# Performance work log

Measured on AMD Instinct MI355X. Metric: run time of the kernel, lower is better.

The kernel has to match this reference:

```python
import jax, jax.numpy as jnp
import numpy as np

B, T, D = 4, 256, 256
H, DK = 4, 64
NUM_REL = 64
EPS = 1e-5


def setup_inputs() -> dict:
    key = jax.random.key(0)
    ks = jax.random.split(key, 16)
    s = 0.02
    return {
        "node_features": jax.random.normal(ks[0], (B, T, D), jnp.float32),
        "spatial_matrix": jax.random.randint(ks[1], (B, T, T), 0, NUM_REL, jnp.int32),
        "Wq": jax.random.normal(ks[2], (D, D), jnp.float32) * s,
        "bq": jnp.zeros((D,), jnp.float32),
        "Wk": jax.random.normal(ks[3], (D, D), jnp.float32) * s,
        "bk": jnp.zeros((D,), jnp.float32),
        "Wv": jax.random.normal(ks[4], (D, D), jnp.float32) * s,
        "bv": jnp.zeros((D,), jnp.float32),
        "rel_k": jax.random.normal(ks[5], (NUM_REL, D), jnp.float32) * s,
        "rel_v": jax.random.normal(ks[6], (NUM_REL, D), jnp.float32) * s,
        "Wo": jax.random.normal(ks[7], (D, D), jnp.float32) * s,
        "bo": jnp.zeros((D,), jnp.float32),
        "gamma": jnp.ones((D,), jnp.float32),
        "beta": jnp.zeros((D,), jnp.float32),
    }


def reference(node_features, spatial_matrix, Wq, bq, Wk, bk, Wv, bv,
              rel_k, rel_v, Wo, bo, gamma, beta):
    b, t, d = node_features.shape
    # projections -> [B,T,H,dk]
    q = (node_features @ Wq.T + bq).reshape(b, t, H, DK)
    k = (node_features @ Wk.T + bk).reshape(b, t, H, DK)
    v = (node_features @ Wv.T + bv).reshape(b, t, H, DK)
    # per-edge relation embeddings -> [B,T,T,H,dk]
    r_k = rel_k[spatial_matrix].reshape(b, t, t, H, DK)
    r_v = rel_v[spatial_matrix].reshape(b, t, t, H, DK)
    # k' = k_j + r_{ij}; scores[b,i,j,h] = <q_i, k'_{ij}> / sqrt(dk)
    k_prime = k[:, None, :, :, :] + r_k
    scores = jnp.einsum('bihd,bijhd->bijh', q, k_prime) / jnp.sqrt(jnp.float32(DK))
    attn = jax.nn.softmax(scores, axis=2)  # over key index j (dropout p used in eval => identity)
    v_prime = v[:, None, :, :, :] + r_v
    agg = jnp.einsum('bijh,bijhd->bihd', attn, v_prime).reshape(b, t, d)
    out = agg @ Wo.T + bo + node_features
    # LayerNorm over last dim
    mu = jnp.mean(out, axis=-1, keepdims=True)
    var = jnp.var(out, axis=-1, keepdims=True)
    out = (out - mu) / jnp.sqrt(var + EPS) * gamma + beta
    return jax.nn.relu(out)
```

## Files before the change

kernel.cpp:

```cpp
#include <hip/hip_runtime.h>

#define TT 256
#define DD 256
#define NH 4
#define DKK 64
#define NR 64
#define NB 4

#define FMA4(A, S, V) { A.x += (S)*(V).x; A.y += (S)*(V).y; A.z += (S)*(V).z; A.w += (S)*(V).w; }

__global__ __launch_bounds__(256) void k_qkv(
    const float* __restrict__ x,
    const float* __restrict__ Wq, const float* __restrict__ bq,
    const float* __restrict__ Wk, const float* __restrict__ bk,
    const float* __restrict__ Wv, const float* __restrict__ bv,
    float* __restrict__ Q, float* __restrict__ K, float* __restrict__ V)
{
    const int z = blockIdx.z;
    const float* __restrict__ W    = (z == 0) ? Wq : (z == 1) ? Wk : Wv;
    const float* __restrict__ bias = (z == 0) ? bq : (z == 1) ? bk : bv;
    float* __restrict__ out        = (z == 0) ? Q  : (z == 1) ? K  : V;
    const int r0 = blockIdx.x * 16, c0 = blockIdx.y * 64;
    __shared__ float xl[16][68];
    __shared__ float wl[64][68];
    const int t = threadIdx.x;
    const int cg = t & 15, rg = t >> 4;
    float acc[4] = {};
    for (int kt = 0; kt < 4; ++kt) {
        const int kb = kt * 64;
        {
            const int r = t >> 4, q4 = t & 15;
            *(float4*)&xl[r][q4 * 4] = *(const float4*)&x[(r0 + r) * DD + kb + q4 * 4];
        }
        #pragma unroll
        for (int u = 0; u < 4; ++u) {
            const int idx = u * 256 + t;
            const int r = idx >> 4, q4 = idx & 15;
            *(float4*)&wl[r][q4 * 4] = *(const float4*)&W[(c0 + r) * DD + kb + q4 * 4];
        }
        __syncthreads();
        #pragma unroll 4
        for (int d4 = 0; d4 < 64; d4 += 4) {
            const float4 xv = *(const float4*)&xl[rg][d4];
            #pragma unroll
            for (int c = 0; c < 4; ++c) {
                const float4 wv = *(const float4*)&wl[cg + 16 * c][d4];
                acc[c] += xv.x * wv.x + xv.y * wv.y + xv.z * wv.z + xv.w * wv.w;
            }
        }
        __syncthreads();
    }
    const int r = r0 + rg;
    #pragma unroll
    for (int c = 0; c < 4; ++c) {
        const int cc = c0 + cg + 16 * c;
        out[r * DD + cc] = acc[c] + bias[cc];
    }
}

__global__ __launch_bounds__(256) void k_attn(
    const float* __restrict__ Q, const float* __restrict__ K, const float* __restrict__ V,
    const int* __restrict__ SM,
    const float* __restrict__ relk, const float* __restrict__ relv,
    float* __restrict__ AGG)
{
    const int it = blockIdx.x, h = blockIdx.y, b = blockIdx.z;
    const int i0 = it * 16;
    __shared__ float ql[16][68];
    __shared__ unsigned char smlp[16][256];
    __shared__ float sl[16][260];
    __shared__ float qrl[16][64];
    __shared__ float wlh[16][64];
    __shared__ float aggp[4][16][68];

    const int t = threadIdx.x;

    {
        const int r = t >> 4, q4 = t & 15;
        *(float4*)&ql[r][q4 * 4] = *(const float4*)&Q[(b * TT + i0 + r) * DD + h * DKK + q4 * 4];
    }
    #pragma unroll
    for (int u = 0; u < 4; ++u) {
        const int idx = u * 256 + t;
        const int i = idx >> 6, j4 = idx & 63;
        const int4 s4 = *(const int4*)&SM[(b * TT + i0 + i) * TT + j4 * 4];
        const unsigned int pk = (unsigned int)(s4.x & 255) | ((unsigned int)(s4.y & 255) << 8)
                              | ((unsigned int)(s4.z & 255) << 16) | ((unsigned int)(s4.w & 255) << 24);
        *(unsigned int*)&smlp[i][j4 * 4] = pk;
    }
    {
        float* wf = &wlh[0][0];
        wf[t] = 0.f; wf[t + 256] = 0.f; wf[t + 512] = 0.f; wf[t + 768] = 0.f;
    }
    __syncthreads();

    {
        const int r = t & 63, ig = t >> 6;
        const float* __restrict__ rk = &relk[r * DD + h * DKK];
        float a0 = 0.f, a1 = 0.f, a2 = 0.f, a3 = 0.f;
        #pragma unroll 4
        for (int d4 = 0; d4 < 64; d4 += 4) {
            const float4 rk4 = *(const float4*)&rk[d4];
            const float4 q0 = *(const float4*)&ql[ig * 4 + 0][d4];
            const float4 q1 = *(const float4*)&ql[ig * 4 + 1][d4];
            const float4 q2 = *(const float4*)&ql[ig * 4 + 2][d4];
            const float4 q3 = *(const float4*)&ql[ig * 4 + 3][d4];
            a0 += q0.x * rk4.x + q0.y * rk4.y + q0.z * rk4.z + q0.w * rk4.w;
            a1 += q1.x * rk4.x + q1.y * rk4.y + q1.z * rk4.z + q1.w * rk4.w;
            a2 += q2.x * rk4.x + q2.y * rk4.y + q2.z * rk4.z + q2.w * rk4.w;
            a3 += q3.x * rk4.x + q3.y * rk4.y + q3.z * rk4.z + q3.w * rk4.w;
        }
        qrl[ig * 4 + 0][r] = a0;
        qrl[ig * 4 + 1][r] = a1;
        qrl[ig * 4 + 2][r] = a2;
        qrl[ig * 4 + 3][r] = a3;
    }
    __syncthreads();

    {
        const int j = t;
        const float* __restrict__ kro = &K[(b * TT + j) * DD + h * DKK];
        float4 kr[16];
        #pragma unroll
        for (int c = 0; c < 16; ++c) kr[c] = *(const float4*)&kro[c * 4];
        for (int i = 0; i < 16; ++i) {
            float a = 0.f;
            #pragma unroll
            for (int c = 0; c < 16; ++c) {
                const float4 q4 = *(const float4*)&ql[i][c * 4];
                a += q4.x * kr[c].x + q4.y * kr[c].y + q4.z * kr[c].z + q4.w * kr[c].w;
            }
            sl[i][j] = (a + qrl[i][smlp[i][j]]) * 0.125f;
        }
    }
    __syncthreads();

    {
        const int row = t >> 4, g = t & 15;
        float vals[16];
        float m = -1e30f;
        #pragma unroll
        for (int jj = 0; jj < 16; ++jj) {
            vals[jj] = sl[row][g + jj * 16];
            m = fmaxf(m, vals[jj]);
        }
        #pragma unroll
        for (int off = 8; off; off >>= 1) m = fmaxf(m, __shfl_xor(m, off, 16));
        float s = 0.f;
        #pragma unroll
        for (int jj = 0; jj < 16; ++jj) { vals[jj] = __expf(vals[jj] - m); s += vals[jj]; }
        #pragma unroll
        for (int off = 8; off; off >>= 1) s += __shfl_xor(s, off, 16);
        const float inv = 1.0f / s;
        #pragma unroll
        for (int jj = 0; jj < 16; ++jj) {
            const float p = vals[jj] * inv;
            sl[row][g + jj * 16] = p;
            atomicAdd(&wlh[row][smlp[row][g + jj * 16]], p);
        }
    }
    __syncthreads();

    {
        const int w = t >> 6, l = t & 63;
        const int dg = l & 15, ig = l >> 4;
        const int jb = w * 64;
        float4 a0 = {0,0,0,0}, a1 = {0,0,0,0}, a2 = {0,0,0,0}, a3 = {0,0,0,0};
        for (int c8 = 0; c8 < 8; ++c8) {
            const int j0 = jb + c8 * 8;
            float4 vr[8];
            #pragma unroll
            for (int u = 0; u < 8; ++u)
                vr[u] = *(const float4*)&V[(b * TT + j0 + u) * DD + h * DKK + dg * 4];
            #pragma unroll
            for (int ii = 0; ii < 4; ++ii) {
                const int i = ig * 4 + ii;
                const float4 pa = *(const float4*)&sl[i][j0];
                const float4 pb = *(const float4*)&sl[i][j0 + 4];
                float4& A = (ii == 0) ? a0 : (ii == 1) ? a1 : (ii == 2) ? a2 : a3;
                FMA4(A, pa.x, vr[0]); FMA4(A, pa.y, vr[1]);
                FMA4(A, pa.z, vr[2]); FMA4(A, pa.w, vr[3]);
                FMA4(A, pb.x, vr[4]); FMA4(A, pb.y, vr[5]);
                FMA4(A, pb.z, vr[6]); FMA4(A, pb.w, vr[7]);
            }
        }
        *(float4*)&aggp[w][ig * 4 + 0][dg * 4] = a0;
        *(float4*)&aggp[w][ig * 4 + 1][dg * 4] = a1;
        *(float4*)&aggp[w][ig * 4 + 2][dg * 4] = a2;
        *(float4*)&aggp[w][ig * 4 + 3][dg * 4] = a3;
    }
    __syncthreads();

    {
        const int d = t & 63, g4 = t >> 6;
        const int ia = g4 * 4;
        float a0 = aggp[0][ia+0][d] + aggp[1][ia+0][d] + aggp[2][ia+0][d] + aggp[3][ia+0][d];
        float a1 = aggp[0][ia+1][d] + aggp[1][ia+1][d] + aggp[2][ia+1][d] + aggp[3][ia+1][d];
        float a2 = aggp[0][ia+2][d] + aggp[1][ia+2][d] + aggp[2][ia+2][d] + aggp[3][ia+2][d];
        float a3 = aggp[0][ia+3][d] + aggp[1][ia+3][d] + aggp[2][ia+3][d] + aggp[3][ia+3][d];
        #pragma unroll 4
        for (int r = 0; r < 64; ++r) {
            const float rv = relv[r * DD + h * DKK + d];
            a0 += wlh[ia + 0][r] * rv;
            a1 += wlh[ia + 1][r] * rv;
            a2 += wlh[ia + 2][r] * rv;
            a3 += wlh[ia + 3][r] * rv;
        }
        AGG[(b * TT + i0 + ia + 0) * DD + h * DKK + d] = a0;
        AGG[(b * TT + i0 + ia + 1) * DD + h * DKK + d] = a1;
        AGG[(b * TT + i0 + ia + 2) * DD + h * DKK + d] = a2;
        AGG[(b * TT + i0 + ia + 3) * DD + h * DKK + d] = a3;
    }
}

__global__ __launch_bounds__(256) void k_oproj(
    const float* __restrict__ AGG, const float* __restrict__ Wo,
    const float* __restrict__ bo, const float* __restrict__ x,
    float* __restrict__ OPRE)
{
    const int r0 = blockIdx.x * 16, c0 = blockIdx.y * 64;
    __shared__ float al[16][68];
    __shared__ float wl[64][68];
    const int t = threadIdx.x;
    const int cg = t & 15, rg = t >> 4;
    float acc[4] = {};
    for (int kt = 0; kt < 4; ++kt) {
        const int kb = kt * 64;
        {
            const int r = t >> 4, q4 = t & 15;
            *(float4*)&al[r][q4 * 4] = *(const float4*)&AGG[(r0 + r) * DD + kb + q4 * 4];
        }
        #pragma unroll
        for (int u = 0; u < 4; ++u) {
            const int idx = u * 256 + t;
            const int r = idx >> 4, q4 = idx & 15;
            *(float4*)&wl[r][q4 * 4] = *(const float4*)&Wo[(c0 + r) * DD + kb + q4 * 4];
        }
        __syncthreads();
        #pragma unroll 4
        for (int d4 = 0; d4 < 64; d4 += 4) {
            const float4 av = *(const float4*)&al[rg][d4];
            #pragma unroll
            for (int c = 0; c < 4; ++c) {
                const float4 wv = *(const float4*)&wl[cg + 16 * c][d4];
                acc[c] += av.x * wv.x + av.y * wv.y + av.z * wv.z + av.w * wv.w;
            }
        }
        __syncthreads();
    }
    const int r = r0 + rg;
    #pragma unroll
    for (int c = 0; c < 4; ++c) {
        const int cc = c0 + cg + 16 * c;
        OPRE[r * DD + cc] = acc[c] + bo[cc] + x[r * DD + cc];
    }
}

__global__ __launch_bounds__(256) void k_ln(
    const float* __restrict__ OPRE, const float* __restrict__ gamma,
    const float* __restrict__ beta, float* __restrict__ out)
{
    const int row = blockIdx.x * 4 + (threadIdx.x >> 6);
    const int lane = threadIdx.x & 63;
    const float4 v = *(const float4*)&OPRE[row * DD + lane * 4];
    float s  = v.x + v.y + v.z + v.w;
    float sq = v.x * v.x + v.y * v.y + v.z * v.z + v.w * v.w;
    #pragma unroll
    for (int off = 32; off; off >>= 1) {
        s  += __shfl_xor(s, off, 64);
        sq += __shfl_xor(sq, off, 64);
    }
    const float mu   = s * (1.0f / DD);
    const float rstd = rsqrtf(sq * (1.0f / DD) - mu * mu + 1e-5f);
    const float4 g  = *(const float4*)&gamma[lane * 4];
    const float4 bt = *(const float4*)&beta[lane * 4];
    float4 o;
    o.x = fmaxf((v.x - mu) * rstd * g.x + bt.x, 0.f);
    o.y = fmaxf((v.y - mu) * rstd * g.y + bt.y, 0.f);
    o.z = fmaxf((v.z - mu) * rstd * g.z + bt.z, 0.f);
    o.w = fmaxf((v.w - mu) * rstd * g.w + bt.w, 0.f);
    *(float4*)&out[row * DD + lane * 4] = o;
}

extern "C" void kernel_launch(void* const* d_in, const int* in_sizes, int n_in,
                              void* d_out, int out_size, void* d_ws, size_t ws_size,
                              hipStream_t stream)
{
    (void)in_sizes; (void)n_in; (void)out_size; (void)ws_size;
    const float* x     = (const float*)d_in[0];
    const int*   SM    = (const int*)d_in[1];
    const float* Wq    = (const float*)d_in[2];
    const float* bq    = (const float*)d_in[3];
    const float* Wk    = (const float*)d_in[4];
    const float* bk    = (const float*)d_in[5];
    const float* Wv    = (const float*)d_in[6];
    const float* bv    = (const float*)d_in[7];
    const float* relk  = (const float*)d_in[8];
    const float* relv  = (const float*)d_in[9];
    const float* Wo    = (const float*)d_in[10];
    const float* bo    = (const float*)d_in[11];
    const float* gamma = (const float*)d_in[12];
    const float* beta  = (const float*)d_in[13];
    float* out = (float*)d_out;
    float* ws  = (float*)d_ws;

    const int NTD = NB * TT * DD;
    float* Q  = ws;
    float* K  = ws + NTD;
    float* V  = ws + 2 * NTD;
    float* AG = ws + 3 * NTD;
    float* OP = ws + 4 * NTD;

    k_qkv  <<<dim3(64, 4, 3), 256, 0, stream>>>(x, Wq, bq, Wk, bk, Wv, bv, Q, K, V);
    k_attn <<<dim3(16, NH, NB), 256, 0, stream>>>(Q, K, V, SM, relk, relv, AG);
    k_oproj<<<dim3(64, 4), 256, 0, stream>>>(AG, Wo, bo, x, OP);
    k_ln   <<<256, 256, 0, stream>>>(OP, gamma, beta, out);
}
```

Before: 135.3 us.

## Stage K, V and rel_k tiles in swizzled shared memory inside attention kernel

```diff
diff --git a/kernel.cpp b/kernel.cpp
--- a/kernel.cpp
+++ b/kernel.cpp
@@ -8,6 +8,7 @@
 #define NB 4
 
 #define FMA4(A, S, V) { A.x += (S)*(V).x; A.y += (S)*(V).y; A.z += (S)*(V).z; A.w += (S)*(V).w; }
+#define DOT4(Q4, K4) ((Q4).x*(K4).x + (Q4).y*(K4).y + (Q4).z*(K4).z + (Q4).w*(K4).w)
 
 __global__ __launch_bounds__(256) void k_qkv(
     const float* __restrict__ x,
@@ -45,7 +46,7 @@
             #pragma unroll
             for (int c = 0; c < 4; ++c) {
                 const float4 wv = *(const float4*)&wl[cg + 16 * c][d4];
-                acc[c] += xv.x * wv.x + xv.y * wv.y + xv.z * wv.z + xv.w * wv.w;
+                acc[c] += DOT4(xv, wv);
             }
         }
         __syncthreads();
@@ -66,14 +67,15 @@
 {
     const int it = blockIdx.x, h = blockIdx.y, b = blockIdx.z;
     const int i0 = it * 16;
-    __shared__ float ql[16][68];
-    __shared__ unsigned char smlp[16][256];
+    __shared__ float kch[64][64];
+    __shared__ float ql[16][64];
     __shared__ float sl[16][260];
     __shared__ float qrl[16][64];
     __shared__ float wlh[16][64];
-    __shared__ float aggp[4][16][68];
+    __shared__ unsigned char smlp[16][256];
 
     const int t = threadIdx.x;
+    #define KCHP(r, k) (&kch[(r)][((((k) + ((r) >> 3)) & 15)) * 4])
 
     {
         const int r = t >> 4, q4 = t & 15;
@@ -94,21 +96,54 @@
     }
     __syncthreads();
 
+    for (int c = 0; c < 4; ++c) {
+        #pragma unroll
+        for (int u = 0; u < 4; ++u) {
+            const int idx = u * 256 + t;
+            const int r = idx >> 4, q4 = idx & 15;
+            *(float4*)KCHP(r, q4) = *(const float4*)&K[(b * TT + c * 64 + r) * DD + h * DKK + q4 * 4];
+        }
+        __syncthreads();
+        {
+            const int jl = t & 63, ig = t >> 6;
+            float a0 = 0.f, a1 = 0.f, a2 = 0.f, a3 = 0.f;
+            #pragma unroll 4
+            for (int d4 = 0; d4 < 64; d4 += 4) {
+                const float4 k4 = *(const float4*)KCHP(jl, d4 >> 2);
+                const float4 q0 = *(const float4*)&ql[ig * 4 + 0][d4];
+                const float4 q1 = *(const float4*)&ql[ig * 4 + 1][d4];
+                const float4 q2 = *(const float4*)&ql[ig * 4 + 2][d4];
+                const float4 q3 = *(const float4*)&ql[ig * 4 + 3][d4];
+                a0 += DOT4(q0, k4); a1 += DOT4(q1, k4);
+                a2 += DOT4(q2, k4); a3 += DOT4(q3, k4);
+            }
+            sl[ig * 4 + 0][c * 64 + jl] = a0;
+            sl[ig * 4 + 1][c * 64 + jl] = a1;
+            sl[ig * 4 + 2][c * 64 + jl] = a2;
+            sl[ig * 4 + 3][c * 64 + jl] = a3;
+        }
+        __syncthreads();
+    }
+
+    #pragma unroll
+    for (int u = 0; u < 4; ++u) {
+        const int idx = u * 256 + t;
+        const int r = idx >> 4, q4 = idx & 15;
+        *(float4*)KCHP(r, q4) = *(const float4*)&relk[r * DD + h * DKK + q4 * 4];
+    }
+    __syncthreads();
     {
         const int r = t & 63, ig = t >> 6;
-        const float* __restrict__ rk = &relk[r * DD + h * DKK];
         float a0 = 0.f, a1 = 0.f, a2 = 0.f, a3 = 0.f;
         #pragma unroll 4
         for (int d4 = 0; d4 < 64; d4 += 4) {
-            const float4 rk4 = *(const float4*)&rk[d4];
+            const float4 rk4 = *(const float4*)KCHP(r, d4 >> 2);
             const float4 q0 = *(const float4*)&ql[ig * 4 + 0][d4];
             const float4 q1 = *(const float4*)&ql[ig * 4 + 1][d4];
             const float4 q2 = *(const float4*)&ql[ig * 4 + 2][d4];
             const float4 q3 = *(const float4*)&ql[ig * 4 + 3][d4];
-            a0 += q0.x * rk4.x + q0.y * rk4.y + q0.z * rk4.z + q0.w * rk4.w;
-            a1 += q1.x * rk4.x + q1.y * rk4.y + q1.z * rk4.z + q1.w * rk4.w;
-            a2 += q2.x * rk4.x + q2.y * rk4.y + q2.z * rk4.z + q2.w * rk4.w;
-            a3 += q3.x * rk4.x + q3.y * rk4.y + q3.z * rk4.z + q3.w * rk4.w;
+            a0 += DOT4(q0, rk4); a1 += DOT4(q1, rk4);
+            a2 += DOT4(q2, rk4); a3 += DOT4(q3, rk4);
         }
         qrl[ig * 4 + 0][r] = a0;
         qrl[ig * 4 + 1][r] = a1;
@@ -118,30 +153,13 @@
     __syncthreads();
 
     {
-        const int j = t;
-        const float* __restrict__ kro = &K[(b * TT + j) * DD + h * DKK];
-        float4 kr[16];
-        #pragma unroll
-        for (int c = 0; c < 16; ++c) kr[c] = *(const float4*)&kro[c * 4];
-        for (int i = 0; i < 16; ++i) {
-            float a = 0.f;
-            #pragma unroll
-            for (int c = 0; c < 16; ++c) {
-                const float4 q4 = *(const float4*)&ql[i][c * 4];
-                a += q4.x * kr[c].x + q4.y * kr[c].y + q4.z * kr[c].z + q4.w * kr[c].w;
-            }
-            sl[i][j] = (a + qrl[i][smlp[i][j]]) * 0.125f;
-        }
-    }
-    __syncthreads();
-
-    {
         const int row = t >> 4, g = t & 15;
         float vals[16];
         float m = -1e30f;
         #pragma unroll
         for (int jj = 0; jj < 16; ++jj) {
-            vals[jj] = sl[row][g + jj * 16];
+            const int j = g + jj * 16;
+            vals[jj] = (sl[row][j] + qrl[row][smlp[row][j]]) * 0.125f;
             m = fmaxf(m, vals[jj]);
         }
         #pragma unroll
@@ -154,63 +172,47 @@
         const float inv = 1.0f / s;
         #pragma unroll
         for (int jj = 0; jj < 16; ++jj) {
+            const int j = g + jj * 16;
             const float p = vals[jj] * inv;
-            sl[row][g + jj * 16] = p;
-            atomicAdd(&wlh[row][smlp[row][g + jj * 16]], p);
+            sl[row][j] = p;
+            atomicAdd(&wlh[row][smlp[row][j]], p);
         }
     }
     __syncthreads();
 
-    {
-        const int w = t >> 6, l = t & 63;
-        const int dg = l & 15, ig = l >> 4;
-        const int jb = w * 64;
-        float4 a0 = {0,0,0,0}, a1 = {0,0,0,0}, a2 = {0,0,0,0}, a3 = {0,0,0,0};
-        for (int c8 = 0; c8 < 8; ++c8) {
-            const int j0 = jb + c8 * 8;
-            float4 vr[8];
-            #pragma unroll
-            for (int u = 0; u < 8; ++u)
-                vr[u] = *(const float4*)&V[(b * TT + j0 + u) * DD + h * DKK + dg * 4];
-            #pragma unroll
-            for (int ii = 0; ii < 4; ++ii) {
-                const int i = ig * 4 + ii;
-                const float4 pa = *(const float4*)&sl[i][j0];
-                const float4 pb = *(const float4*)&sl[i][j0 + 4];
-                float4& A = (ii == 0) ? a0 : (ii == 1) ? a1 : (ii == 2) ? a2 : a3;
-                FMA4(A, pa.x, vr[0]); FMA4(A, pa.y, vr[1]);
-                FMA4(A, pa.z, vr[2]); FMA4(A, pa.w, vr[3]);
-                FMA4(A, pb.x, vr[4]); FMA4(A, pb.y, vr[5]);
-                FMA4(A, pb.z, vr[6]); FMA4(A, pb.w, vr[7]);
-            }
-        }
-        *(float4*)&aggp[w][ig * 4 + 0][dg * 4] = a0;
-        *(float4*)&aggp[w][ig * 4 + 1][dg * 4] = a1;
-        *(float4*)&aggp[w][ig * 4 + 2][dg * 4] = a2;
-        *(float4*)&aggp[w][ig * 4 + 3][dg * 4] = a3;
-    }
-    __syncthreads();
-
-    {
-        const int d = t & 63, g4 = t >> 6;
-        const int ia = g4 * 4;
-        float a0 = aggp[0][ia+0][d] + aggp[1][ia+0][d] + aggp[2][ia+0][d] + aggp[3][ia+0][d];
-        float a1 = aggp[0][ia+1][d] + aggp[1][ia+1][d] + aggp[2][ia+1][d] + aggp[3][ia+1][d];
-        float a2 = aggp[0][ia+2][d] + aggp[1][ia+2][d] + aggp[2][ia+2][d] + aggp[3][ia+2][d];
-        float a3 = aggp[0][ia+3][d] + aggp[1][ia+3][d] + aggp[2][ia+3][d] + aggp[3][ia+3][d];
+    const int w5 = t >> 6, l5 = t & 63;
+    const int dg = l5 & 15, ig5 = l5 >> 4;
+    const int i5 = w5 * 4 + ig5;
+    float4 acc = {0.f, 0.f, 0.f, 0.f};
+    for (int c = 0; c < 4; ++c) {
+        #pragma unroll
+        for (int u = 0; u < 4; ++u) {
+            const int idx = u * 256 + t;
+            const int r = idx >> 4, q4 = idx & 15;
+            *(float4*)KCHP(r, q4) = *(const float4*)&V[(b * TT + c * 64 + r) * DD + h * DKK + q4 * 4];
+        }
+        __syncthreads();
+        #pragma unroll 4
+        for (int jl = 0; jl < 64; jl += 4) {
+            const float4 p4 = *(const float4*)&sl[i5][c * 64 + jl];
+            FMA4(acc, p4.x, *(const float4*)KCHP(jl + 0, dg));
+            FMA4(acc, p4.y, *(const float4*)KCHP(jl + 1, dg));
+            FMA4(acc, p4.z, *(const float4*)KCHP(jl + 2, dg));
+            FMA4(acc, p4.w, *(const float4*)KCHP(jl + 3, dg));
+        }
+        __syncthreads();
+    }
+
+    {
         #pragma unroll 4
         for (int r = 0; r < 64; ++r) {
-            const float rv = relv[r * DD + h * DKK + d];
-            a0 += wlh[ia + 0][r] * rv;
-            a1 += wlh[ia + 1][r] * rv;
-            a2 += wlh[ia + 2][r] * rv;
-            a3 += wlh[ia + 3][r] * rv;
-        }
-        AGG[(b * TT + i0 + ia + 0) * DD + h * DKK + d] = a0;
-        AGG[(b * TT + i0 + ia + 1) * DD + h * DKK + d] = a1;
-        AGG[(b * TT + i0 + ia + 2) * DD + h * DKK + d] = a2;
-        AGG[(b * TT + i0 + ia + 3) * DD + h * DKK + d] = a3;
-    }
+            const float wv = wlh[i5][r];
+            const float4 rv = *(const float4*)&relv[r * DD + h * DKK + dg * 4];
+            FMA4(acc, wv, rv);
+        }
+        *(float4*)&AGG[(b * TT + i0 + i5) * DD + h * DKK + dg * 4] = acc;
+    }
+    #undef KCHP
 }
 
 __global__ __launch_bounds__(256) void k_oproj(
@@ -243,7 +245,7 @@
             #pragma unroll
             for (int c = 0; c < 4; ++c) {
                 const float4 wv = *(const float4*)&wl[cg + 16 * c][d4];
-                acc[c] += av.x * wv.x + av.y * wv.y + av.z * wv.z + av.w * wv.w;
+                acc[c] += DOT4(av, wv);
             }
         }
         __syncthreads();
```

Measured after the change: 136.3 us. No clear change (+0.8%).
